# Kernel optimization log

Hardware: AMD Instinct MI355X
Metric: run time of the kernel (lower is better)

Reference implementation:

```python
import jax, jax.numpy as jnp
import numpy as np

N_HEAD, D_MODEL, DQ, DK, DV = 16, 1024, 64, 64, 64
B, LQ, LK = 2, 2048, 2048
EPS = 1e-3


def setup_inputs() -> dict:
    key = jax.random.key(0)
    ks = jax.random.split(key, 8)
    v = jax.random.normal(ks[0], (B, LK, D_MODEL), jnp.float32)
    k = jax.random.normal(ks[1], (B, LK, D_MODEL), jnp.float32)
    q = jax.random.normal(ks[2], (B, LQ, D_MODEL), jnp.float32)
    mask = jax.random.randint(ks[3], (B, LQ, LK), 0, 2).astype(bool)
    # xavier_normal for [n_head, d_model, d*]: fan_in=d_model, fan_out=d* (per torch, last two dims)
    def xav(kk, shape):
        std = np.sqrt(2.0 / (shape[-2] + shape[-1]))
        return jax.random.normal(kk, shape, jnp.float32) * std
    w_q = xav(ks[4], (N_HEAD, D_MODEL, DQ))
    w_k = xav(ks[5], (N_HEAD, D_MODEL, DK))
    w_v = xav(ks[6], (N_HEAD, D_MODEL, DV))
    # output linear: torch default init; use uniform(-1/sqrt(fan_in), ..)
    fan_in = N_HEAD * DV
    bound = 1.0 / np.sqrt(fan_in)
    kw, kb = jax.random.split(ks[7])
    w_o = jax.random.uniform(kw, (fan_in, D_MODEL), jnp.float32, -bound, bound)
    b_o = jax.random.uniform(kb, (D_MODEL,), jnp.float32, -bound, bound)
    gamma = jnp.ones((D_MODEL,), jnp.float32)
    beta = jnp.zeros((D_MODEL,), jnp.float32)
    return {"v": v, "k": k, "q": q, "mask": mask, "w_q": w_q, "w_k": w_k,
            "w_v": w_v, "w_o": w_o, "b_o": b_o, "gamma": gamma, "beta": beta}


def _layer_norm(x, gamma, beta):
    mean = jnp.mean(x, axis=-1, keepdims=True)
    # torch.std default is unbiased (ddof=1); eps added to std (not var)
    std = jnp.std(x, axis=-1, keepdims=True, ddof=1)
    return (x - mean) / (std + EPS) * gamma + beta


def reference(v, k, q, mask, w_q, w_k, w_v, w_o, b_o, gamma, beta):
    residual = k  # source uses k as residual
    # per-head projections: [h, b, l, d*]
    qh = jnp.einsum('bld,hde->hble', q, w_q)
    kh = jnp.einsum('bld,hde->hble', k, w_k)
    vh = jnp.einsum('bld,hde->hble', v, w_v)
    scale = 1.0 / np.sqrt(DK)
    scores = jnp.einsum('hbqe,hbke->hbqk', qh, kh) * scale  # [h,b,Lq,Lk]
    scores = jnp.where(mask[None], -jnp.inf, scores)
    attn = jax.nn.softmax(scores, axis=-1)
    out = jnp.einsum('hbqk,hbke->hbqe', attn, vh)  # [h,b,Lq,dv]
    # cat(split(out, batch, dim=0), dim=-1): heads concatenated on last dim
    out = out.transpose(1, 2, 0, 3).reshape(out.shape[1], out.shape[2], -1)
    out = out @ w_o + b_o
    x = out + residual  # dropout is identity in eval
    return _layer_norm(x, gamma, beta)
```

## Files before the change

kernel.cpp:

```cpp
#include <hip/hip_runtime.h>
#include <math.h>

typedef __bf16 bf16_t;
typedef bf16_t bf16x8 __attribute__((ext_vector_type(8)));
typedef float  f32x4  __attribute__((ext_vector_type(4)));
typedef unsigned short u16;
typedef u16 ushortx4 __attribute__((ext_vector_type(4)));
typedef unsigned long long u64;

#define MFMA16(a, b, c) __builtin_amdgcn_mfma_f32_16x16x32_bf16((a), (b), (c), 0, 0, 0)

__device__ __forceinline__ u16 f2bf(float f) {
    unsigned int u = __float_as_uint(f);
    u = (u + 0x7fffu + ((u >> 16) & 1u)) >> 16;
    return (u16)u;
}

__device__ __forceinline__ void gld16(const u16* g, u16* l) {
    __builtin_amdgcn_global_load_lds(
        (const __attribute__((address_space(1))) void*)g,
        (__attribute__((address_space(3))) void*)l, 16, 0, 0);
}


__global__ __launch_bounds__(256) void k_cvt3(const float* __restrict__ q,
                                              const float* __restrict__ k,
                                              const float* __restrict__ v,
                                              u16* __restrict__ qb,
                                              u16* __restrict__ kb,
                                              u16* __restrict__ vb) {
    int i = blockIdx.x * 256 + threadIdx.x;
    int sel = blockIdx.y;
    const float* src = sel == 0 ? q : (sel == 1 ? k : v);
    u16* dst = sel == 0 ? qb : (sel == 1 ? kb : vb);
    float4 val = ((const float4*)src)[i];
    ushortx4 r;
    r[0] = f2bf(val.x); r[1] = f2bf(val.y); r[2] = f2bf(val.z); r[3] = f2bf(val.w);
    ((ushortx4*)dst)[i] = r;
}

__global__ __launch_bounds__(256) void k_tcvt3(const float* __restrict__ w_q,
                                               const float* __restrict__ w_k,
                                               const float* __restrict__ w_v,
                                               u16* __restrict__ wqt,
                                               u16* __restrict__ wkt,
                                               u16* __restrict__ wvt) {
    __shared__ float tile[32][33];
    int z = blockIdx.z, h = z & 15, sel = z >> 4;
    const float* src = (sel == 0 ? w_q : (sel == 1 ? w_k : w_v));
    u16* dst = (sel == 0 ? wqt : (sel == 1 ? wkt : wvt));
    int r0 = blockIdx.x * 32, c0 = blockIdx.y * 32;
    int tx = threadIdx.x & 31, ty = threadIdx.x >> 5;
    const float* s = src + ((size_t)h * 1024 + r0) * 64 + c0;
#pragma unroll
    for (int i = 0; i < 4; ++i) tile[ty + i * 8][tx] = s[(ty + i * 8) * 64 + tx];
    __syncthreads();
    u16* d = dst + ((size_t)h * 64 + c0) * 1024 + r0;
#pragma unroll
    for (int i = 0; i < 4; ++i) d[(ty + i * 8) * 1024 + tx] = f2bf(tile[tx][ty + i * 8]);
}

__global__ __launch_bounds__(256) void k_tcvt(const float* __restrict__ src,
                                              u16* __restrict__ dst, int R, int C) {
    __shared__ float tile[32][33];
    int r0 = blockIdx.x * 32, c0 = blockIdx.y * 32;
    int tx = threadIdx.x & 31, ty = threadIdx.x >> 5;
    const float* s = src + (size_t)r0 * C + c0;
#pragma unroll
    for (int i = 0; i < 4; ++i) tile[ty + i * 8][tx] = s[(ty + i * 8) * (size_t)C + tx];
    __syncthreads();
    u16* d = dst + (size_t)c0 * R + r0;
#pragma unroll
    for (int i = 0; i < 4; ++i) d[(ty + i * 8) * (size_t)R + tx] = f2bf(tile[tx][ty + i * 8]);
}

__global__ __launch_bounds__(256) void k_packmask(const int* __restrict__ mask,
                                                  u64* __restrict__ mask64) {
    int bid = blockIdx.x;
    int ktg = bid & 7, q4 = (bid >> 3) & 511, b = bid >> 12;
    int wave = threadIdx.x >> 6, lane = threadIdx.x & 63;
    int q = q4 * 4 + wave;
    const int* mp = mask + ((size_t)(b * 2048 + q)) * 2048 + ktg * 256 + lane;
#pragma unroll
    for (int i = 0; i < 4; ++i) {
        int m = mp[i * 64];
        u64 bal = __ballot(m != 0);
        if (lane == 0) mask64[((size_t)(b * 32 + ktg * 4 + i)) * 2048 + q] = bal;
    }
}

#define GEMM_CORE(Ablk, Bblk, ACC)                                                    \
    int c0 = wave * 2;                                                                \
    const u16* Ag0 = Ablk + (size_t)(c0 * 16 + l15) * 1024 + quad * 8;                \
    const u16* Ag1 = Ablk + (size_t)((c0 + 1) * 16 + l15) * 1024 + quad * 8;          \
    const u16* Bg0 = Bblk + (size_t)(c0 * 16 + l15) * 1024 + quad * 8;                \
    const u16* Bg1 = Bblk + (size_t)((c0 + 1) * 16 + l15) * 1024 + quad * 8;          \
    gld16(Ag0, As + c0 * 512); gld16(Ag1, As + (c0 + 1) * 512);                       \
    gld16(Bg0, Bs + c0 * 512); gld16(Bg1, Bs + (c0 + 1) * 512);                       \
    __syncthreads();                                                                  \
    int buf = 0;                                                                      \
    for (int ks = 0; ks < 32; ++ks) {                                                 \
        if (ks < 31) {                                                                \
            int k0 = (ks + 1) * 32;                                                   \
            gld16(Ag0 + k0, As + (buf ^ 1) * 4096 + c0 * 512);                        \
            gld16(Ag1 + k0, As + (buf ^ 1) * 4096 + (c0 + 1) * 512);                  \
            gld16(Bg0 + k0, Bs + (buf ^ 1) * 4096 + c0 * 512);                        \
            gld16(Bg1 + k0, Bs + (buf ^ 1) * 4096 + (c0 + 1) * 512);                  \
        }                                                                             \
        bf16x8 af[4], bfr[4];                                                         \
        _Pragma("unroll")                                                             \
        for (int i = 0; i < 4; ++i)                                                   \
            af[i] = *(const bf16x8*)(As + buf * 4096 + (wy * 4 + i) * 512 + lane * 8);\
        _Pragma("unroll")                                                             \
        for (int j = 0; j < 4; ++j)                                                   \
            bfr[j] = *(const bf16x8*)(Bs + buf * 4096 + (wx * 4 + j) * 512 + lane * 8);\
        _Pragma("unroll")                                                             \
        for (int i = 0; i < 4; ++i)                                                   \
            _Pragma("unroll")                                                         \
            for (int j = 0; j < 4; ++j) ACC[i][j] = MFMA16(af[i], bfr[j], ACC[i][j]); \
        __syncthreads();                                                              \
        buf ^= 1;                                                                     \
    }

__global__ __launch_bounds__(256) void k_proj(
    const u16* __restrict__ qb, const u16* __restrict__ kb, const u16* __restrict__ vb,
    const u16* __restrict__ wqt, const u16* __restrict__ wkt, const u16* __restrict__ wvt,
    u16* __restrict__ oq, u16* __restrict__ okh, u16* __restrict__ ovt) {
    __shared__ __align__(16) u16 smem[18432];
    u16* As = smem;
    u16* Bs = smem + 8192;
    int z = blockIdx.y, gx = blockIdx.x;
    int bm, bn;
    const u16 *A, *B;
    if (z == 0)      { bm = gx >> 3; bn = gx & 7; A = qb; B = wqt; }
    else if (z == 1) { bm = gx >> 3; bn = gx & 7; A = kb; B = wkt; }
    else             { bm = gx & 7; bn = gx >> 3; A = wvt; B = vb; }
    A += (size_t)bm * 128 * 1024;
    B += (size_t)bn * 128 * 1024;
    int tid = threadIdx.x, wave = tid >> 6, lane = tid & 63;
    int wy = wave >> 1, wx = wave & 1, l15 = lane & 15, quad = lane >> 4;
    f32x4 acc[4][4] = {};
    GEMM_CORE(A, B, acc)
    u16* ep = smem + wave * 4608;
    float mulf = (z == 0) ? 0.18033688011112042f : 1.0f;
#pragma unroll
    for (int i = 0; i < 4; ++i)
#pragma unroll
        for (int j = 0; j < 4; ++j)
#pragma unroll
            for (int r = 0; r < 4; ++r)
                ep[(i * 16 + quad * 4 + r) * 72 + j * 16 + l15] = f2bf(acc[i][j][r] * mulf);
    int rl = lane >> 3, cg = lane & 7;
    if (z < 2) {
        int hh = bn * 2 + wx;
        int m0 = bm * 128 + wy * 64;
        int bb = m0 >> 11, l0 = m0 & 2047;
        u16* O = (z ? okh : oq) + ((size_t)((hh * 2 + bb) * 2048 + l0)) * 64;
#pragma unroll
        for (int s = 0; s < 8; ++s) {
            int row = s * 8 + rl;
            uint4 v = *(const uint4*)(ep + row * 72 + cg * 8);
            *(uint4*)(O + (size_t)row * 64 + cg * 8) = v;
        }
    } else {
        int m0 = bm * 128 + wy * 64;
        int hh = m0 >> 6;
        int n0 = bn * 128 + wx * 64;
        int bb = n0 >> 11, l0 = n0 & 2047;
        u16* O = ovt + (size_t)(hh * 2 + bb) * 131072 + (size_t)(m0 & 63) * 2048 + l0;
#pragma unroll
        for (int s = 0; s < 8; ++s) {
            int row = s * 8 + rl;
            uint4 v = *(const uint4*)(ep + row * 72 + cg * 8);
            *(uint4*)(O + (size_t)row * 2048 + cg * 8) = v;
        }
    }
}

__global__ __launch_bounds__(256) void k_out(
    const u16* __restrict__ ao, const u16* __restrict__ wot,
    const float* __restrict__ bo, const float* __restrict__ resid,
    float* __restrict__ xb) {
    __shared__ __align__(16) u16 smem[18432];
    u16* As = smem;
    u16* Bs = smem + 8192;
    int gx = blockIdx.x, bm = gx >> 3, bn = gx & 7;
    const u16* A = ao + (size_t)bm * 128 * 1024;
    const u16* B = wot + (size_t)bn * 128 * 1024;
    int tid = threadIdx.x, wave = tid >> 6, lane = tid & 63;
    int wy = wave >> 1, wx = wave & 1, l15 = lane & 15, quad = lane >> 4;
    f32x4 acc[4][4] = {};
    GEMM_CORE(A, B, acc)
    float* epf = (float*)(smem) + wave * 2176;
    int cgf = lane & 15, rlf = lane >> 4;
    int mbase = bm * 128 + wy * 64, nbase = bn * 128 + wx * 64;
#pragma unroll
    for (int cc = 0; cc < 2; ++cc) {
#pragma unroll
        for (int i2 = 0; i2 < 2; ++i2)
#pragma unroll
            for (int j = 0; j < 4; ++j)
#pragma unroll
                for (int r = 0; r < 4; ++r)
                    epf[(i2 * 16 + quad * 4 + r) * 68 + j * 16 + l15] =
                        acc[cc * 2 + i2][j][r];
#pragma unroll
        for (int s = 0; s < 8; ++s) {
            int row = s * 4 + rlf;
            f32x4 v = *(const f32x4*)(epf + row * 68 + cgf * 4);
            int m = mbase + cc * 32 + row, n = nbase + cgf * 4;
            float4 rsd = *(const float4*)(resid + (size_t)m * 1024 + n);
            float4 bo4 = *(const float4*)(bo + n);
            float4 o;
            o.x = v[0] + bo4.x + rsd.x;
            o.y = v[1] + bo4.y + rsd.y;
            o.z = v[2] + bo4.z + rsd.z;
            o.w = v[3] + bo4.w + rsd.w;
            *(float4*)(xb + (size_t)m * 1024 + n) = o;
        }
    }
}

__global__ __launch_bounds__(256) void k_attn(
    const u16* __restrict__ qh, const u16* __restrict__ kh,
    const u16* __restrict__ vt, const u64* __restrict__ mask64,
    u16* __restrict__ ao) {
    int qt = blockIdx.x, hb = blockIdx.y;
    int h = hb >> 1, b = hb & 1;
    int tid = threadIdx.x, wave = tid >> 6, lane = tid & 63;
    int l15 = lane & 15, quad = lane >> 4;

    __shared__ __align__(16) u16 Ks[2][4096], Vs[2][4096];
    __shared__ __align__(16) u16 Pb[4][2][16][72];

    int qrow0 = qt * 128 + wave * 32;
    const u16* Qp = qh + ((size_t)(hb * 2048) + qrow0 + l15) * 64 + quad * 8;
    bf16x8 qf[2][2];
    qf[0][0] = *(const bf16x8*)Qp;
    qf[0][1] = *(const bf16x8*)(Qp + 32);
    qf[1][0] = *(const bf16x8*)(Qp + 1024);
    qf[1][1] = *(const bf16x8*)(Qp + 1024 + 32);

    int c0 = wave * 2;
    int rA = (c0 >> 1) * 16 + l15, dA = (c0 & 1) * 32 + quad * 8;
    int rB = ((c0 + 1) >> 1) * 16 + l15, dB = ((c0 + 1) & 1) * 32 + quad * 8;
    const u16* Kg0 = kh + (size_t)hb * 131072 + (size_t)rA * 64 + dA;
    const u16* Kg1 = kh + (size_t)hb * 131072 + (size_t)rB * 64 + dB;
    const u16* Vg0 = vt + (size_t)hb * 131072 + (size_t)rA * 2048 + dA;
    const u16* Vg1 = vt + (size_t)hb * 131072 + (size_t)rB * 2048 + dB;
    const u64* Mp = mask64 + (size_t)b * 65536 + qrow0 + l15;

    float l_lane[2] = {0.f, 0.f};
    f32x4 o[2][4] = {};

    gld16(Kg0, &Ks[0][c0 * 512]);
    gld16(Kg1, &Ks[0][(c0 + 1) * 512]);
    gld16(Vg0, &Vs[0][c0 * 512]);
    gld16(Vg1, &Vs[0][(c0 + 1) * 512]);
    u64 mw0 = Mp[0], mw1 = Mp[16];
    __syncthreads();
    int buf = 0;
    for (int kt = 0; kt < 32; ++kt) {
        u64 mwn0 = 0, mwn1 = 0;
        if (kt < 31) {
            gld16(Kg0 + (size_t)(kt + 1) * 4096, &Ks[buf ^ 1][c0 * 512]);
            gld16(Kg1 + (size_t)(kt + 1) * 4096, &Ks[buf ^ 1][(c0 + 1) * 512]);
            gld16(Vg0 + (size_t)(kt + 1) * 64, &Vs[buf ^ 1][c0 * 512]);
            gld16(Vg1 + (size_t)(kt + 1) * 64, &Vs[buf ^ 1][(c0 + 1) * 512]);
            mwn0 = Mp[(size_t)(kt + 1) * 2048];
            mwn1 = Mp[(size_t)(kt + 1) * 2048 + 16];
        }
        bf16x8 kf[8], vf[8];
#pragma unroll
        for (int c = 0; c < 8; ++c) kf[c] = *(const bf16x8*)&Ks[buf][c * 512 + lane * 8];
#pragma unroll
        for (int c = 0; c < 8; ++c) vf[c] = *(const bf16x8*)&Vs[buf][c * 512 + lane * 8];
#pragma unroll
        for (int hf = 0; hf < 2; ++hf) {
            u64 mw = hf ? mw1 : mw0;
            f32x4 st[4] = {};
#pragma unroll
            for (int t = 0; t < 4; ++t) {
                st[t] = MFMA16(kf[t * 2], qf[hf][0], st[t]);
                st[t] = MFMA16(kf[t * 2 + 1], qf[hf][1], st[t]);
            }
            unsigned int w0 = (unsigned int)(mw >> (quad * 4));
            unsigned int w1 = (unsigned int)(mw >> (32 + quad * 4));
#pragma unroll
            for (int r = 0; r < 4; ++r) {
                st[0][r] = ((w0 >> r) & 1u) ? -3e30f : st[0][r];
                st[1][r] = ((w0 >> (16 + r)) & 1u) ? -3e30f : st[1][r];
                st[2][r] = ((w1 >> r) & 1u) ? -3e30f : st[2][r];
                st[3][r] = ((w1 >> (16 + r)) & 1u) ? -3e30f : st[3][r];
            }
            float ll = 0.f;
#pragma unroll
            for (int t = 0; t < 4; ++t) {
                float p0 = __builtin_amdgcn_exp2f(st[t][0]);
                float p1 = __builtin_amdgcn_exp2f(st[t][1]);
                float p2 = __builtin_amdgcn_exp2f(st[t][2]);
                float p3 = __builtin_amdgcn_exp2f(st[t][3]);
                ll += (p0 + p1) + (p2 + p3);
                uint2 pk;
                pk.x = (__float_as_uint(p1) & 0xffff0000u) | (__float_as_uint(p0) >> 16);
                pk.y = (__float_as_uint(p3) & 0xffff0000u) | (__float_as_uint(p2) >> 16);
                *(uint2*)&Pb[wave][hf][l15][t * 16 + quad * 4] = pk;
            }
            l_lane[hf] += ll;
#pragma unroll
            for (int kc = 0; kc < 2; ++kc) {
                bf16x8 pf = *(const bf16x8*)&Pb[wave][hf][l15][kc * 32 + quad * 8];
#pragma unroll
                for (int t = 0; t < 4; ++t)
                    o[hf][t] = MFMA16(pf, vf[t * 2 + kc], o[hf][t]);
            }
        }
        mw0 = mwn0; mw1 = mwn1;
        __syncthreads();
        buf ^= 1;
    }
#pragma unroll
    for (int hf = 0; hf < 2; ++hf) {
        float ls = l_lane[hf];
        ls += __shfl_xor(ls, 16, 64);
        ls += __shfl_xor(ls, 32, 64);
        float inv = 1.0f / ls;
        f32x4 ivr;
#pragma unroll
        for (int r = 0; r < 4; ++r) ivr[r] = __shfl(inv, quad * 4 + r, 16);
#pragma unroll
        for (int t = 0; t < 4; ++t)
#pragma unroll
            for (int r = 0; r < 4; ++r)
                Pb[wave][hf][quad * 4 + r][t * 16 + l15] = f2bf(o[hf][t][r] * ivr[r]);
    }
    int rl = lane >> 3, cg = lane & 7;
#pragma unroll
    for (int hf = 0; hf < 2; ++hf)
#pragma unroll
        for (int s = 0; s < 2; ++s) {
            int row = s * 8 + rl;
            uint4 v = *(const uint4*)&Pb[wave][hf][row][cg * 8];
            *(uint4*)(ao + ((size_t)(b * 2048 + qrow0 + hf * 16 + row)) * 1024 +
                      h * 64 + cg * 8) = v;
        }
}

__global__ __launch_bounds__(256) void k_ln(const float* __restrict__ x,
                                            const float* __restrict__ gamma,
                                            const float* __restrict__ beta,
                                            float* __restrict__ out) {
    int row = blockIdx.x;
    const float* xr = x + (size_t)row * 1024;
    float4 v = ((const float4*)xr)[threadIdx.x];
    float s = v.x + v.y + v.z + v.w;
    float ss = v.x * v.x + v.y * v.y + v.z * v.z + v.w * v.w;
#pragma unroll
    for (int off = 32; off; off >>= 1) {
        s += __shfl_down(s, off, 64);
        ss += __shfl_down(ss, off, 64);
    }
    __shared__ float sb[8];
    int wave = threadIdx.x >> 6, lane = threadIdx.x & 63;
    if (lane == 0) { sb[wave] = s; sb[4 + wave] = ss; }
    __syncthreads();
    s = sb[0] + sb[1] + sb[2] + sb[3];
    ss = sb[4] + sb[5] + sb[6] + sb[7];
    float mean = s * (1.0f / 1024.0f);
    float var = fmaxf((ss - 1024.0f * mean * mean) * (1.0f / 1023.0f), 0.f);
    float inv = 1.0f / (sqrtf(var) + 1e-3f);
    float4 g = ((const float4*)gamma)[threadIdx.x];
    float4 bt = ((const float4*)beta)[threadIdx.x];
    float4 o;
    o.x = (v.x - mean) * inv * g.x + bt.x;
    o.y = (v.y - mean) * inv * g.y + bt.y;
    o.z = (v.z - mean) * inv * g.z + bt.z;
    o.w = (v.w - mean) * inv * g.w + bt.w;
    ((float4*)(out + (size_t)row * 1024))[threadIdx.x] = o;
}

extern "C" void kernel_launch(void* const* d_in, const int* in_sizes, int n_in,
                              void* d_out, int out_size, void* d_ws, size_t ws_size,
                              hipStream_t stream) {
    const float* v_in  = (const float*)d_in[0];
    const float* k_in  = (const float*)d_in[1];
    const float* q_in  = (const float*)d_in[2];
    const int*   mask  = (const int*)d_in[3];
    const float* w_q   = (const float*)d_in[4];
    const float* w_k   = (const float*)d_in[5];
    const float* w_v   = (const float*)d_in[6];
    const float* w_o   = (const float*)d_in[7];
    const float* b_o   = (const float*)d_in[8];
    const float* gamma = (const float*)d_in[9];
    const float* beta  = (const float*)d_in[10];
    float* out = (float*)d_out;

    char* ws = (char*)d_ws;
    const size_t MB = 1ull << 20;
    u16* qb  = (u16*)(ws + 0 * MB);
    u16* kb  = (u16*)(ws + 8 * MB);
    u16* vb  = (u16*)(ws + 16 * MB);
    u16* wqt = (u16*)(ws + 24 * MB);
    u16* wkt = (u16*)(ws + 26 * MB);
    u16* wvt = (u16*)(ws + 28 * MB);
    u16* wot = (u16*)(ws + 30 * MB);
    u16* qh  = (u16*)(ws + 32 * MB);
    u16* kh  = (u16*)(ws + 40 * MB);
    u16* vt  = (u16*)(ws + 48 * MB);
    u16* ao  = (u16*)(ws + 56 * MB);
    u64* mask64 = (u64*)(ws + 64 * MB);
    float* xb = (float*)(ws + 64 * MB);

    k_cvt3<<<dim3(4096, 3), dim3(256), 0, stream>>>(q_in, k_in, v_in, qb, kb, vb);
    k_tcvt3<<<dim3(32, 2, 48), dim3(256), 0, stream>>>(w_q, w_k, w_v, wqt, wkt, wvt);
    k_tcvt<<<dim3(32, 32), dim3(256), 0, stream>>>(w_o, wot, 1024, 1024);
    k_packmask<<<dim3(8192), dim3(256), 0, stream>>>(mask, mask64);
    k_proj<<<dim3(256, 3), dim3(256), 0, stream>>>(qb, kb, vb, wqt, wkt, wvt, qh, kh, vt);
    k_attn<<<dim3(16, 32), dim3(256), 0, stream>>>(qh, kh, vt, mask64, ao);
    k_out<<<dim3(256), dim3(256), 0, stream>>>(ao, wot, b_o, k_in, xb);
    k_ln<<<dim3(4096), dim3(256), 0, stream>>>(xb, gamma, beta, out);
}
```

Before: 308.1 us.

## Split attention over key halves with merge kernel and widen out-GEMM to 8 waves

The attention kernel now runs 512-thread blocks over 256 query rows and splits the key range into two halves via a grid z dimension. Each block writes unnormalized bf16 partial outputs and row sums, and a new merge kernel adds the halves, normalizes and writes the head-concatenated layout. The output projection GEMM moves to 512 threads with an inline 4x2 wave tiling instead of the shared GEMM core. The goal is more waves in flight per block and better occupancy, at the cost of an extra kernel launch, extra global traffic for the partials, and an extra bf16 rounding of the partial sums.

```diff
diff --git a/kernel.cpp b/kernel.cpp
--- a/kernel.cpp
+++ b/kernel.cpp
@@ -14,6 +14,10 @@
     unsigned int u = __float_as_uint(f);
     u = (u + 0x7fffu + ((u >> 16) & 1u)) >> 16;
     return (u16)u;
+}
+
+__device__ __forceinline__ float bf2f(unsigned int u) {
+    return __uint_as_float(u << 16);
 }
 
 __device__ __forceinline__ void gld16(const u16* g, u16* l) {
@@ -177,7 +181,7 @@
     }
 }
 
-__global__ __launch_bounds__(256) void k_out(
+__global__ __launch_bounds__(512) void k_out(
     const u16* __restrict__ ao, const u16* __restrict__ wot,
     const float* __restrict__ bo, const float* __restrict__ resid,
     float* __restrict__ xb) {
@@ -188,27 +192,52 @@
     const u16* A = ao + (size_t)bm * 128 * 1024;
     const u16* B = wot + (size_t)bn * 128 * 1024;
     int tid = threadIdx.x, wave = tid >> 6, lane = tid & 63;
-    int wy = wave >> 1, wx = wave & 1, l15 = lane & 15, quad = lane >> 4;
-    f32x4 acc[4][4] = {};
-    GEMM_CORE(A, B, acc)
-    float* epf = (float*)(smem) + wave * 2176;
-    int cgf = lane & 15, rlf = lane >> 4;
-    int mbase = bm * 128 + wy * 64, nbase = bn * 128 + wx * 64;
+    int wy = wave >> 2, wx = wave & 3, l15 = lane & 15, quad = lane >> 4;
+    const u16* Ag = A + (size_t)(wave * 16 + l15) * 1024 + quad * 8;
+    const u16* Bg = B + (size_t)(wave * 16 + l15) * 1024 + quad * 8;
+    f32x4 acc[4][2] = {};
+    gld16(Ag, As + wave * 512);
+    gld16(Bg, Bs + wave * 512);
+    __syncthreads();
+    int buf = 0;
+    for (int ks = 0; ks < 32; ++ks) {
+        if (ks < 31) {
+            int k0 = (ks + 1) * 32;
+            gld16(Ag + k0, As + (buf ^ 1) * 4096 + wave * 512);
+            gld16(Bg + k0, Bs + (buf ^ 1) * 4096 + wave * 512);
+        }
+        bf16x8 af[4], bfr[2];
+#pragma unroll
+        for (int i = 0; i < 4; ++i)
+            af[i] = *(const bf16x8*)(As + buf * 4096 + (wy * 4 + i) * 512 + lane * 8);
+#pragma unroll
+        for (int j = 0; j < 2; ++j)
+            bfr[j] = *(const bf16x8*)(Bs + buf * 4096 + (wx * 2 + j) * 512 + lane * 8);
+#pragma unroll
+        for (int i = 0; i < 4; ++i)
+#pragma unroll
+            for (int j = 0; j < 2; ++j) acc[i][j] = MFMA16(af[i], bfr[j], acc[i][j]);
+        __syncthreads();
+        buf ^= 1;
+    }
+    float* epf = (float*)smem + wave * 1152;
+    int rl = lane >> 3, cg = lane & 7;
+    int mbase = bm * 128 + wy * 64, nbase = bn * 128 + wx * 32;
 #pragma unroll
     for (int cc = 0; cc < 2; ++cc) {
 #pragma unroll
         for (int i2 = 0; i2 < 2; ++i2)
 #pragma unroll
-            for (int j = 0; j < 4; ++j)
+            for (int j = 0; j < 2; ++j)
 #pragma unroll
                 for (int r = 0; r < 4; ++r)
-                    epf[(i2 * 16 + quad * 4 + r) * 68 + j * 16 + l15] =
+                    epf[(i2 * 16 + quad * 4 + r) * 36 + j * 16 + l15] =
                         acc[cc * 2 + i2][j][r];
 #pragma unroll
-        for (int s = 0; s < 8; ++s) {
-            int row = s * 4 + rlf;
-            f32x4 v = *(const f32x4*)(epf + row * 68 + cgf * 4);
-            int m = mbase + cc * 32 + row, n = nbase + cgf * 4;
+        for (int s = 0; s < 4; ++s) {
+            int row = s * 8 + rl;
+            f32x4 v = *(const f32x4*)(epf + row * 36 + cg * 4);
+            int m = mbase + cc * 32 + row, n = nbase + cg * 4;
             float4 rsd = *(const float4*)(resid + (size_t)m * 1024 + n);
             float4 bo4 = *(const float4*)(bo + n);
             float4 o;
@@ -221,19 +250,19 @@
     }
 }
 
-__global__ __launch_bounds__(256) void k_attn(
+__global__ __launch_bounds__(512) void k_attn(
     const u16* __restrict__ qh, const u16* __restrict__ kh,
     const u16* __restrict__ vt, const u64* __restrict__ mask64,
-    u16* __restrict__ ao) {
-    int qt = blockIdx.x, hb = blockIdx.y;
-    int h = hb >> 1, b = hb & 1;
+    u16* __restrict__ po, float* __restrict__ pl) {
+    int qt = blockIdx.x, hb = blockIdx.y, ksp = blockIdx.z;
+    int b = hb & 1;
     int tid = threadIdx.x, wave = tid >> 6, lane = tid & 63;
     int l15 = lane & 15, quad = lane >> 4;
 
     __shared__ __align__(16) u16 Ks[2][4096], Vs[2][4096];
-    __shared__ __align__(16) u16 Pb[4][2][16][72];
-
-    int qrow0 = qt * 128 + wave * 32;
+    __shared__ __align__(16) u16 Pb[8][16][72];
+
+    int qrow0 = qt * 256 + wave * 32;
     const u16* Qp = qh + ((size_t)(hb * 2048) + qrow0 + l15) * 64 + quad * 8;
     bf16x8 qf[2][2];
     qf[0][0] = *(const bf16x8*)Qp;
@@ -241,32 +270,24 @@
     qf[1][0] = *(const bf16x8*)(Qp + 1024);
     qf[1][1] = *(const bf16x8*)(Qp + 1024 + 32);
 
-    int c0 = wave * 2;
-    int rA = (c0 >> 1) * 16 + l15, dA = (c0 & 1) * 32 + quad * 8;
-    int rB = ((c0 + 1) >> 1) * 16 + l15, dB = ((c0 + 1) & 1) * 32 + quad * 8;
-    const u16* Kg0 = kh + (size_t)hb * 131072 + (size_t)rA * 64 + dA;
-    const u16* Kg1 = kh + (size_t)hb * 131072 + (size_t)rB * 64 + dB;
-    const u16* Vg0 = vt + (size_t)hb * 131072 + (size_t)rA * 2048 + dA;
-    const u16* Vg1 = vt + (size_t)hb * 131072 + (size_t)rB * 2048 + dB;
-    const u64* Mp = mask64 + (size_t)b * 65536 + qrow0 + l15;
+    int rC = (wave >> 1) * 16 + l15, dC = (wave & 1) * 32 + quad * 8;
+    const u16* Kg = kh + (size_t)hb * 131072 + (size_t)ksp * 65536 + (size_t)rC * 64 + dC;
+    const u16* Vg = vt + (size_t)hb * 131072 + (size_t)rC * 2048 + ksp * 1024 + dC;
+    const u64* Mp = mask64 + (size_t)b * 65536 + (size_t)ksp * 32768 + qrow0 + l15;
 
     float l_lane[2] = {0.f, 0.f};
     f32x4 o[2][4] = {};
 
-    gld16(Kg0, &Ks[0][c0 * 512]);
-    gld16(Kg1, &Ks[0][(c0 + 1) * 512]);
-    gld16(Vg0, &Vs[0][c0 * 512]);
-    gld16(Vg1, &Vs[0][(c0 + 1) * 512]);
+    gld16(Kg, &Ks[0][wave * 512]);
+    gld16(Vg, &Vs[0][wave * 512]);
     u64 mw0 = Mp[0], mw1 = Mp[16];
     __syncthreads();
     int buf = 0;
-    for (int kt = 0; kt < 32; ++kt) {
+    for (int kt = 0; kt < 16; ++kt) {
         u64 mwn0 = 0, mwn1 = 0;
-        if (kt < 31) {
-            gld16(Kg0 + (size_t)(kt + 1) * 4096, &Ks[buf ^ 1][c0 * 512]);
-            gld16(Kg1 + (size_t)(kt + 1) * 4096, &Ks[buf ^ 1][(c0 + 1) * 512]);
-            gld16(Vg0 + (size_t)(kt + 1) * 64, &Vs[buf ^ 1][c0 * 512]);
-            gld16(Vg1 + (size_t)(kt + 1) * 64, &Vs[buf ^ 1][(c0 + 1) * 512]);
+        if (kt < 15) {
+            gld16(Kg + (size_t)(kt + 1) * 4096, &Ks[buf ^ 1][wave * 512]);
+            gld16(Vg + (size_t)(kt + 1) * 64, &Vs[buf ^ 1][wave * 512]);
             mwn0 = Mp[(size_t)(kt + 1) * 2048];
             mwn1 = Mp[(size_t)(kt + 1) * 2048 + 16];
         }
@@ -304,12 +325,12 @@
                 uint2 pk;
                 pk.x = (__float_as_uint(p1) & 0xffff0000u) | (__float_as_uint(p0) >> 16);
                 pk.y = (__float_as_uint(p3) & 0xffff0000u) | (__float_as_uint(p2) >> 16);
-                *(uint2*)&Pb[wave][hf][l15][t * 16 + quad * 4] = pk;
+                *(uint2*)&Pb[wave][l15][t * 16 + quad * 4] = pk;
             }
             l_lane[hf] += ll;
 #pragma unroll
             for (int kc = 0; kc < 2; ++kc) {
-                bf16x8 pf = *(const bf16x8*)&Pb[wave][hf][l15][kc * 32 + quad * 8];
+                bf16x8 pf = *(const bf16x8*)&Pb[wave][l15][kc * 32 + quad * 8];
 #pragma unroll
                 for (int t = 0; t < 4; ++t)
                     o[hf][t] = MFMA16(pf, vf[t * 2 + kc], o[hf][t]);
@@ -319,31 +340,54 @@
         __syncthreads();
         buf ^= 1;
     }
+    size_t rowbase = ((size_t)ksp * 32 + hb) * 2048 + qrow0;
+    int rl = lane >> 3, cg = lane & 7;
 #pragma unroll
     for (int hf = 0; hf < 2; ++hf) {
         float ls = l_lane[hf];
         ls += __shfl_xor(ls, 16, 64);
         ls += __shfl_xor(ls, 32, 64);
-        float inv = 1.0f / ls;
-        f32x4 ivr;
-#pragma unroll
-        for (int r = 0; r < 4; ++r) ivr[r] = __shfl(inv, quad * 4 + r, 16);
+        if (quad == 0) pl[rowbase + hf * 16 + l15] = ls;
 #pragma unroll
         for (int t = 0; t < 4; ++t)
 #pragma unroll
             for (int r = 0; r < 4; ++r)
-                Pb[wave][hf][quad * 4 + r][t * 16 + l15] = f2bf(o[hf][t][r] * ivr[r]);
-    }
-    int rl = lane >> 3, cg = lane & 7;
-#pragma unroll
-    for (int hf = 0; hf < 2; ++hf)
+                Pb[wave][quad * 4 + r][t * 16 + l15] = f2bf(o[hf][t][r]);
 #pragma unroll
         for (int s = 0; s < 2; ++s) {
             int row = s * 8 + rl;
-            uint4 v = *(const uint4*)&Pb[wave][hf][row][cg * 8];
-            *(uint4*)(ao + ((size_t)(b * 2048 + qrow0 + hf * 16 + row)) * 1024 +
-                      h * 64 + cg * 8) = v;
-        }
+            uint4 v = *(const uint4*)&Pb[wave][row][cg * 8];
+            *(uint4*)(po + (rowbase + hf * 16 + row) * 64 + cg * 8) = v;
+        }
+    }
+}
+
+__global__ __launch_bounds__(256) void k_amerge(const u16* __restrict__ po,
+                                                const float* __restrict__ pl,
+                                                u16* __restrict__ ao) {
+    int bid = blockIdx.x;
+    int hb = bid >> 6, rc = bid & 63;
+    int h = hb >> 1, b = hb & 1;
+    int tid = threadIdx.x;
+    int r = tid >> 3, c = tid & 7;
+    int row = rc * 32 + r;
+    size_t i0 = ((size_t)hb * 2048 + row) * 64 + c * 8;
+    uint4 a0 = *(const uint4*)(po + i0);
+    uint4 a1 = *(const uint4*)(po + i0 + 4194304);
+    float l0 = pl[(size_t)hb * 2048 + row];
+    float l1 = pl[65536 + (size_t)hb * 2048 + row];
+    float inv = 1.0f / (l0 + l1);
+    unsigned int* pa0 = (unsigned int*)&a0;
+    unsigned int* pa1 = (unsigned int*)&a1;
+    uint4 out;
+    unsigned int* po_ = (unsigned int*)&out;
+#pragma unroll
+    for (int i = 0; i < 4; ++i) {
+        float lo = (bf2f(pa0[i] & 0xffffu) + bf2f(pa1[i] & 0xffffu)) * inv;
+        float hi = (bf2f(pa0[i] >> 16) + bf2f(pa1[i] >> 16)) * inv;
+        po_[i] = (unsigned int)f2bf(lo) | ((unsigned int)f2bf(hi) << 16);
+    }
+    *(uint4*)(ao + ((size_t)(b * 2048 + row)) * 1024 + h * 64 + c * 8) = out;
 }
 
 __global__ __launch_bounds__(256) void k_ln(const float* __restrict__ x,
@@ -410,13 +454,16 @@
     u16* ao  = (u16*)(ws + 56 * MB);
     u64* mask64 = (u64*)(ws + 64 * MB);
     float* xb = (float*)(ws + 64 * MB);
+    u16*   po = (u16*)(ws + 0 * MB);
+    float* pl = (float*)(ws + 16 * MB);
 
     k_cvt3<<<dim3(4096, 3), dim3(256), 0, stream>>>(q_in, k_in, v_in, qb, kb, vb);
     k_tcvt3<<<dim3(32, 2, 48), dim3(256), 0, stream>>>(w_q, w_k, w_v, wqt, wkt, wvt);
     k_tcvt<<<dim3(32, 32), dim3(256), 0, stream>>>(w_o, wot, 1024, 1024);
     k_packmask<<<dim3(8192), dim3(256), 0, stream>>>(mask, mask64);
     k_proj<<<dim3(256, 3), dim3(256), 0, stream>>>(qb, kb, vb, wqt, wkt, wvt, qh, kh, vt);
-    k_attn<<<dim3(16, 32), dim3(256), 0, stream>>>(qh, kh, vt, mask64, ao);
-    k_out<<<dim3(256), dim3(256), 0, stream>>>(ao, wot, b_o, k_in, xb);
+    k_attn<<<dim3(8, 32, 2), dim3(512), 0, stream>>>(qh, kh, vt, mask64, po, pl);
+    k_amerge<<<dim3(2048), dim3(256), 0, stream>>>(po, pl, ao);
+    k_out<<<dim3(256), dim3(512), 0, stream>>>(ao, wot, b_o, k_in, xb);
     k_ln<<<dim3(4096), dim3(256), 0, stream>>>(xb, gamma, beta, out);
 }
```

Measured after the change: 311.4 us. No clear change (+1.1%).
